# Kernel optimization log

Measured on AMD Instinct MI355X. Metric: run time of the kernel, lower is better.

Reference implementation:

```python
import jax, jax.numpy as jnp
import numpy as np

EMBED_DIM = 1024
NUM_HEADS = 16
NUM_KV_HEADS = 4
HEAD_DIM = 64
WINDOW_SIZE = 32
TOKENS_PER_FRAME = 64
BASE_T, BASE_D, BASE_B = 10000.0, 100.0, 100.0


def apply_3d_rope(x, pos_t, pos_d, pos_b):
    # x: (B, S, H, D); pos_*: (S,) int
    D = x.shape[-1]
    half = D // 2
    dim_idx = jnp.arange(half, dtype=jnp.float32)
    inv_freq = 1.0 / (BASE_T ** (2.0 * dim_idx / D))  # (half,)
    ang = (pos_t.astype(jnp.float32)[:, None] * inv_freq
           + pos_d.astype(jnp.float32)[:, None] * inv_freq * (BASE_T / BASE_D)
           + pos_b.astype(jnp.float32)[:, None] * inv_freq * (BASE_T / BASE_B))  # (S, half)
    cos = jnp.cos(ang)[None, :, None, :]
    sin = jnp.sin(ang)[None, :, None, :]
    x1 = x[..., 0::2]
    x2 = x[..., 1::2]
    y1 = x1 * cos - x2 * sin
    y2 = x1 * sin + x2 * cos
    return jnp.stack([y1, y2], axis=-1).reshape(x.shape)


def setup_inputs() -> dict:
    key = jax.random.key(0)
    ks = jax.random.split(key, 8)
    B, Sn, Lp = 1, 1024, 4096
    hidden_states = jax.random.normal(ks[0], (B, Sn, EMBED_DIM), dtype=jnp.float32)
    past_k = jax.random.normal(ks[1], (B, NUM_KV_HEADS, Lp, HEAD_DIM), dtype=jnp.float32)
    past_v = jax.random.normal(ks[2], (B, NUM_KV_HEADS, Lp, HEAD_DIM), dtype=jnp.float32)
    wq = jax.random.normal(ks[3], (EMBED_DIM, NUM_HEADS * HEAD_DIM), dtype=jnp.float32) * 0.02
    wk = jax.random.normal(ks[4], (EMBED_DIM, NUM_KV_HEADS * HEAD_DIM), dtype=jnp.float32) * 0.02
    wv = jax.random.normal(ks[5], (EMBED_DIM, NUM_KV_HEADS * HEAD_DIM), dtype=jnp.float32) * 0.02
    wo = jax.random.normal(ks[6], (NUM_HEADS * HEAD_DIM, EMBED_DIM), dtype=jnp.float32) * 0.02
    # frame-time positions: tokens_per_frame tokens share a frame time; past frames 0..63, new frames 64..79
    past_idx = jnp.arange(Lp, dtype=jnp.int32)
    new_idx = jnp.arange(Sn, dtype=jnp.int32)
    past_t = past_idx // TOKENS_PER_FRAME
    new_t = new_idx // TOKENS_PER_FRAME + Lp // TOKENS_PER_FRAME
    # 8x8 depth-by-bearing patch grid within each frame
    past_d = (past_idx % TOKENS_PER_FRAME) // 8
    past_b = past_idx % 8
    new_d = (new_idx % TOKENS_PER_FRAME) // 8
    new_b = new_idx % 8
    return dict(hidden_states=hidden_states, past_k=past_k, past_v=past_v,
                wq=wq, wk=wk, wv=wv, wo=wo,
                new_t=new_t, new_d=new_d, new_b=new_b,
                past_t=past_t, past_d=past_d, past_b=past_b)


def reference(hidden_states, past_k, past_v, wq, wk, wv, wo,
              new_t, new_d, new_b, past_t, past_d, past_b):
    B, Sn, _ = hidden_states.shape
    Lp = past_t.shape[0]
    Q = (hidden_states @ wq).reshape(B, Sn, NUM_HEADS, HEAD_DIM)
    Kn = (hidden_states @ wk).reshape(B, Sn, NUM_KV_HEADS, HEAD_DIM)
    Vn = (hidden_states @ wv).reshape(B, Sn, NUM_KV_HEADS, HEAD_DIM)
    Q = apply_3d_rope(Q, new_t, new_d, new_b)
    Kn = apply_3d_rope(Kn, new_t, new_d, new_b)
    Q = Q.transpose(0, 2, 1, 3)   # (B, H, Sn, D)
    Kn = Kn.transpose(0, 2, 1, 3)  # (B, KVH, Sn, D)
    Vn = Vn.transpose(0, 2, 1, 3)
    # Sliding-window truncation on frame time: torch does searchsorted + slice
    # (drop past keys with time < min_time). Masking those keys to -inf is
    # mathematically identical and jit-friendly (static shapes).
    min_time = new_t.max() - (WINDOW_SIZE - 1)
    past_keep = past_t >= min_time                                    # (Lp,)
    valid = jnp.concatenate([past_keep, jnp.ones((Sn,), dtype=bool)])  # (Lp+Sn,)
    pos_t = jnp.concatenate([past_t, new_t])
    K = jnp.concatenate([past_k, Kn], axis=2)  # (B, KVH, Lp+Sn, D)
    V = jnp.concatenate([past_v, Vn], axis=2)
    rep = NUM_HEADS // NUM_KV_HEADS
    K = jnp.repeat(K, rep, axis=1)  # (B, H, L, D) -- repeat_interleave semantics
    V = jnp.repeat(V, rep, axis=1)
    scores = jnp.einsum('bhqd,bhkd->bhqk', Q, K) / jnp.sqrt(jnp.float32(HEAD_DIM))
    mask = (pos_t[None, :] <= new_t[:, None]) & valid[None, :]  # (Sn, L) frame-causal + window
    scores = jnp.where(mask[None, None], scores, jnp.float32(-jnp.inf))
    attn = jax.nn.softmax(scores, axis=-1)
    attn = jnp.nan_to_num(attn)  # fully-masked rows -> 0 (matches torch nan_to_num)
    out = jnp.einsum('bhqk,bhkd->bhqd', attn, V)
    out = out.transpose(0, 2, 1, 3).reshape(B, Sn, NUM_HEADS * HEAD_DIM)
    out = out @ wo
    return out, Kn, Vn
```

## Files before the change

### kernel.cpp

```cpp
#include <hip/hip_runtime.h>
#include <math.h>

#define EMBED 1024
#define NH 16
#define NKV 4
#define HD 64
#define SN 1024
#define LP 4096
#define WIN 32

#define FREQ_C 0.4152410118609203f

typedef float floatx4 __attribute__((ext_vector_type(4)));
typedef __bf16 bf16x8 __attribute__((ext_vector_type(8)));

__global__ __launch_bounds__(256) void prep_kernel(
    const float* __restrict__ hidden, const float* __restrict__ wq,
    const float* __restrict__ wk, const float* __restrict__ wv,
    const float* __restrict__ wo,
    __bf16* __restrict__ hidb, __bf16* __restrict__ wqT,
    __bf16* __restrict__ wkT, __bf16* __restrict__ wvT,
    __bf16* __restrict__ woT)
{
    const int jb = blockIdx.x, tid = threadIdx.x;
    if (jb >= 640) {
        const size_t base = (size_t)(jb - 640) * 4096 + (size_t)tid * 16;
        float4 f0 = *(const float4*)(hidden + base);
        float4 f1 = *(const float4*)(hidden + base + 4);
        float4 f2 = *(const float4*)(hidden + base + 8);
        float4 f3 = *(const float4*)(hidden + base + 12);
        bf16x8 o0, o1;
        o0[0] = (__bf16)f0.x; o0[1] = (__bf16)f0.y;
        o0[2] = (__bf16)f0.z; o0[3] = (__bf16)f0.w;
        o0[4] = (__bf16)f1.x; o0[5] = (__bf16)f1.y;
        o0[6] = (__bf16)f1.z; o0[7] = (__bf16)f1.w;
        o1[0] = (__bf16)f2.x; o1[1] = (__bf16)f2.y;
        o1[2] = (__bf16)f2.z; o1[3] = (__bf16)f2.w;
        o1[4] = (__bf16)f3.x; o1[5] = (__bf16)f3.y;
        o1[6] = (__bf16)f3.z; o1[7] = (__bf16)f3.w;
        *(bf16x8*)(hidb + base) = o0;
        *(bf16x8*)(hidb + base + 8) = o1;
        return;
    }
    const float* src; __bf16* dst; int N, tk, tn;
    if (jb < 256)      { src = wq; dst = wqT; N = 1024; tk = jb >> 4;         tn = jb & 15; }
    else if (jb < 320) { src = wk; dst = wkT; N = 256;  tk = (jb - 256) >> 2; tn = (jb - 256) & 3; }
    else if (jb < 384) { src = wv; dst = wvT; N = 256;  tk = (jb - 320) >> 2; tn = (jb - 320) & 3; }
    else               { src = wo; dst = woT; N = 1024; tk = (jb - 384) >> 4; tn = (jb - 384) & 15; }

    __shared__ float T[64][65];
    {
        const int r = tid >> 2, c0 = (tid & 3) * 16;
        const float* sp = src + (size_t)(tk * 64 + r) * N + tn * 64 + c0;
        float4 v0 = *(const float4*)(sp + 0);
        float4 v1 = *(const float4*)(sp + 4);
        float4 v2 = *(const float4*)(sp + 8);
        float4 v3 = *(const float4*)(sp + 12);
        *(float4*)&T[r][c0 + 0] = v0;
        *(float4*)&T[r][c0 + 4] = v1;
        *(float4*)&T[r][c0 + 8] = v2;
        *(float4*)&T[r][c0 + 12] = v3;
    }
    __syncthreads();
    {
        const int n = tid >> 2, k0 = (tid & 3) * 16;
        bf16x8 o0, o1;
#pragma unroll
        for (int j = 0; j < 8; j++) {
            o0[j] = (__bf16)T[k0 + j][n];
            o1[j] = (__bf16)T[k0 + 8 + j][n];
        }
        __bf16* dp = dst + (size_t)(tn * 64 + n) * 1024 + tk * 64 + k0;
        *(bf16x8*)dp = o0;
        *(bf16x8*)(dp + 8) = o1;
    }
}

__global__ __launch_bounds__(256) void qkv_mfma_kernel(
    const __bf16* __restrict__ hidb, const __bf16* __restrict__ wqT,
    const __bf16* __restrict__ wkT, const __bf16* __restrict__ wvT,
    const int* __restrict__ new_t, const int* __restrict__ new_d,
    const int* __restrict__ new_b,
    float* __restrict__ qws, float* __restrict__ knp, float* __restrict__ vnp)
{
    __shared__ __bf16 ASh[64][72];
    __shared__ __bf16 BSh[64][72];

    const int tid = threadIdx.x;
    const int lane = tid & 63, w = tid >> 6;
    const int g = lane >> 4, c = lane & 15;
    const int bx = blockIdx.x, by = blockIdx.y;

    int mode, cbase;
    const __bf16* W;
    if (bx < 16)      { mode = 0; W = wqT; cbase = bx * 64; }
    else if (bx < 20) { mode = 1; W = wkT; cbase = (bx - 16) * 64; }
    else              { mode = 2; W = wvT; cbase = (bx - 20) * 64; }

    const int arow = tid >> 2, ak = (tid & 3) * 16;
    const __bf16* Ap = hidb + (size_t)(by * 64 + arow) * EMBED + ak;
    const int bn = tid & 63, bk0 = (tid >> 6) * 16;
    const __bf16* Bp = W + (size_t)(cbase + bn) * 1024 + bk0;

    floatx4 acc[4] = {floatx4(0.f), floatx4(0.f), floatx4(0.f), floatx4(0.f)};

    bf16x8 a0 = *(const bf16x8*)(Ap);
    bf16x8 a1 = *(const bf16x8*)(Ap + 8);
    bf16x8 b0 = *(const bf16x8*)(Bp);
    bf16x8 b1 = *(const bf16x8*)(Bp + 8);

    const int strip = w * 16;

    for (int k0 = 0; k0 < EMBED; k0 += 64) {
        __syncthreads();
        *(bf16x8*)&ASh[arow][ak] = a0;
        *(bf16x8*)&ASh[arow][ak + 8] = a1;
        *(bf16x8*)&BSh[bn][bk0] = b0;
        *(bf16x8*)&BSh[bn][bk0 + 8] = b1;
        __syncthreads();
        if (k0 + 64 < EMBED) {
            a0 = *(const bf16x8*)(Ap + k0 + 64);
            a1 = *(const bf16x8*)(Ap + k0 + 72);
            b0 = *(const bf16x8*)(Bp + k0 + 64);
            b1 = *(const bf16x8*)(Bp + k0 + 72);
        }
        bf16x8 af0 = *(const bf16x8*)&ASh[strip + c][g * 8];
        bf16x8 af1 = *(const bf16x8*)&ASh[strip + c][32 + g * 8];
#pragma unroll
        for (int t = 0; t < 4; t++) {
            bf16x8 bf0 = *(const bf16x8*)&BSh[t * 16 + c][g * 8];
            bf16x8 bf1 = *(const bf16x8*)&BSh[t * 16 + c][32 + g * 8];
            acc[t] = __builtin_amdgcn_mfma_f32_16x16x32_bf16(af0, bf0, acc[t], 0, 0, 0);
            acc[t] = __builtin_amdgcn_mfma_f32_16x16x32_bf16(af1, bf1, acc[t], 0, 0, 0);
        }
    }

    const int m0 = strip + g * 4;
    if (mode == 2) {
        const int kvh = bx - 20;
#pragma unroll
        for (int r = 0; r < 4; r++) {
            const int token = by * 64 + m0 + r;
#pragma unroll
            for (int t = 0; t < 4; t++)
                vnp[((size_t)kvh * SN + token) * HD + t * 16 + c] = acc[t][r];
        }
    } else {
        float fr[4];
#pragma unroll
        for (int t = 0; t < 4; t++) {
            const int d = (cbase + t * 16 + c) & 63;
            fr[t] = exp2f(-FREQ_C * (float)(d >> 1));
        }
        const int par = c & 1;
#pragma unroll
        for (int r = 0; r < 4; r++) {
            const int token = by * 64 + m0 + r;
            const float ft = (float)new_t[token];
            const float fdb = (float)(new_d[token] + new_b[token]);
#pragma unroll
            for (int t = 0; t < 4; t++) {
                const float ang = ft * fr[t] + fdb * (fr[t] * 100.0f);
                float sv, cv;
                sincosf(ang, &sv, &cv);
                const float x = acc[t][r];
                const float xp = __shfl_xor(x, 1, 64);
                const float y = par ? (xp * sv + x * cv) : (x * cv - xp * sv);
                if (mode == 0) {
                    qws[(size_t)token * EMBED + cbase + t * 16 + c] = y;
                } else {
                    const int kvh = bx - 16;
                    knp[((size_t)kvh * SN + token) * HD + t * 16 + c] = y;
                }
            }
        }
    }
}

__global__ __launch_bounds__(256) void out_mfma_kernel(
    const __bf16* __restrict__ ctxb, const __bf16* __restrict__ woT,
    float* __restrict__ C)
{
    __shared__ __bf16 ASh[64][72];
    __shared__ __bf16 BSh[64][72];

    const int tid = threadIdx.x;
    const int lane = tid & 63, w = tid >> 6;
    const int g = lane >> 4, c = lane & 15;
    const int bx = blockIdx.x, by = blockIdx.y;

    const int arow = tid >> 2, ak = (tid & 3) * 16;
    const __bf16* Ap = ctxb + (size_t)(by * 64 + arow) * EMBED + ak;
    const int bn = tid & 63, bk0 = (tid >> 6) * 16;
    const __bf16* Bp = woT + (size_t)(bx * 64 + bn) * 1024 + bk0;

    floatx4 acc[4] = {floatx4(0.f), floatx4(0.f), floatx4(0.f), floatx4(0.f)};

    bf16x8 a0 = *(const bf16x8*)(Ap);
    bf16x8 a1 = *(const bf16x8*)(Ap + 8);
    bf16x8 b0 = *(const bf16x8*)(Bp);
    bf16x8 b1 = *(const bf16x8*)(Bp + 8);

    const int strip = w * 16;

    for (int k0 = 0; k0 < EMBED; k0 += 64) {
        __syncthreads();
        *(bf16x8*)&ASh[arow][ak] = a0;
        *(bf16x8*)&ASh[arow][ak + 8] = a1;
        *(bf16x8*)&BSh[bn][bk0] = b0;
        *(bf16x8*)&BSh[bn][bk0 + 8] = b1;
        __syncthreads();
        if (k0 + 64 < EMBED) {
            a0 = *(const bf16x8*)(Ap + k0 + 64);
            a1 = *(const bf16x8*)(Ap + k0 + 72);
            b0 = *(const bf16x8*)(Bp + k0 + 64);
            b1 = *(const bf16x8*)(Bp + k0 + 72);
        }
        bf16x8 af0 = *(const bf16x8*)&ASh[strip + c][g * 8];
        bf16x8 af1 = *(const bf16x8*)&ASh[strip + c][32 + g * 8];
#pragma unroll
        for (int t = 0; t < 4; t++) {
            bf16x8 bf0 = *(const bf16x8*)&BSh[t * 16 + c][g * 8];
            bf16x8 bf1 = *(const bf16x8*)&BSh[t * 16 + c][32 + g * 8];
            acc[t] = __builtin_amdgcn_mfma_f32_16x16x32_bf16(af0, bf0, acc[t], 0, 0, 0);
            acc[t] = __builtin_amdgcn_mfma_f32_16x16x32_bf16(af1, bf1, acc[t], 0, 0, 0);
        }
    }

    const int m0 = strip + g * 4;
#pragma unroll
    for (int r = 0; r < 4; r++) {
        const int row = by * 64 + m0 + r;
#pragma unroll
        for (int t = 0; t < 4; t++)
            C[(size_t)row * EMBED + bx * 64 + t * 16 + c] = acc[t][r];
    }
}

#define PREFETCH_CHUNK(CI)                                                     \
    {                                                                          \
        const int base_ = (myStart + (CI)) << 6;                               \
        const int gk_ = base_ + skk;                                           \
        if (gk_ < Nk) {                                                        \
            const float* kp_ = (gk_ < nPast)                                   \
                ? past_k + ((size_t)(kvh * LP + p0 + gk_)) * HD + sd0          \
                : knp + ((size_t)(kvh * SN + (gk_ - nPast))) * HD + sd0;       \
            kb0 = *(const float4*)(kp_ + 0);                                   \
            kb1 = *(const float4*)(kp_ + 4);                                   \
            kb2 = *(const float4*)(kp_ + 8);                                   \
            kb3 = *(const float4*)(kp_ + 12);                                  \
        } else {                                                               \
            kb0 = kb1 = kb2 = kb3 = make_float4(0.f, 0.f, 0.f, 0.f);           \
        }                                                                      \
        const int gv0_ = base_ + 2 * kp2;                                      \
        if (gv0_ < Nk) {                                                       \
            const float* vp_ = (gv0_ < nPast)                                  \
                ? past_v + ((size_t)(kvh * LP + p0 + gv0_)) * HD + vdb         \
                : vnp + ((size_t)(kvh * SN + (gv0_ - nPast))) * HD + vdb;      \
            vb00 = *(const float4*)(vp_ + 0);                                  \
            vb01 = *(const float4*)(vp_ + 4);                                  \
        } else {                                                               \
            vb00 = vb01 = make_float4(0.f, 0.f, 0.f, 0.f);                     \
        }                                                                      \
        const int gv1_ = gv0_ + 1;                                             \
        if (gv1_ < Nk) {                                                       \
            const float* vp_ = (gv1_ < nPast)                                  \
                ? past_v + ((size_t)(kvh * LP + p0 + gv1_)) * HD + vdb         \
                : vnp + ((size_t)(kvh * SN + (gv1_ - nPast))) * HD + vdb;      \
            vb10 = *(const float4*)(vp_ + 0);                                  \
            vb11 = *(const float4*)(vp_ + 4);                                  \
        } else {                                                               \
            vb10 = vb11 = make_float4(0.f, 0.f, 0.f, 0.f);                     \
        }                                                                      \
        if (tid < 64) {                                                        \
            const int g2_ = base_ + tid;                                       \
            ptreg = (g2_ < Nk)                                                 \
                ? ((g2_ < nPast) ? past_t[p0 + g2_] : new_t[g2_ - nPast])      \
                : 0x7fffffff;                                                  \
        }                                                                      \
    }

__global__ __launch_bounds__(256) void attn_kernel(
    const float* __restrict__ qws, const float* __restrict__ past_k,
    const float* __restrict__ past_v, const float* __restrict__ knp,
    const float* __restrict__ vnp, const int* __restrict__ new_t,
    const int* __restrict__ past_t, float* __restrict__ opart,
    float* __restrict__ lpart)
{
    __shared__ __bf16 KS[64][72];
    __shared__ __bf16 VS[64][72];
    __shared__ __bf16 PS[64][72];
    __shared__ float MSK[64];

    const int tid = threadIdx.x;
    const int i = blockIdx.x;
    const int xcd = i & 7;
    const int kvh = xcd >> 1;
    const int jj = i >> 3;
    const int hloc = jj & 3;
    const int f = (jj >> 2) & 15;
    const int sidx = (xcd & 1) | (((jj >> 6) & 1) << 1);
    const int h = kvh * 4 + hloc;

    const int lane = tid & 63, w = tid >> 6;
    const int g = lane >> 4, c = lane & 15;

    const int tmax = new_t[SN - 1];
    const int min_time = tmax - (WIN - 1);
    const int qtf = new_t[f * 64];

    int lo = 0, hi = LP;
    while (lo < hi) {
        int mid = (lo + hi) >> 1;
        if (past_t[mid] >= min_time) hi = mid; else lo = mid + 1;
    }
    const int p0 = lo;
    const int nPast = LP - p0;
    const int Nk = nPast + (f + 1) * 64;

    const int nch = (Nk + 63) >> 6;
    const int qch = nch >> 2, rem = nch & 3;
    const int myCount = qch + (sidx < rem ? 1 : 0);
    const int myStart = sidx * qch + (sidx < rem ? sidx : rem);

    bf16x8 aQ[2];
    {
        const int q = f * 64 + w * 16 + c;
        const float* qp = qws + (size_t)q * EMBED + h * HD + g * 8;
#pragma unroll
        for (int s = 0; s < 2; s++) {
            float4 q0 = *(const float4*)(qp + s * 32);
            float4 q1 = *(const float4*)(qp + s * 32 + 4);
            bf16x8 a;
            a[0] = (__bf16)q0.x; a[1] = (__bf16)q0.y;
            a[2] = (__bf16)q0.z; a[3] = (__bf16)q0.w;
            a[4] = (__bf16)q1.x; a[5] = (__bf16)q1.y;
            a[6] = (__bf16)q1.z; a[7] = (__bf16)q1.w;
            aQ[s] = a;
        }
    }

    floatx4 oacc[4] = {floatx4(0.f), floatx4(0.f), floatx4(0.f), floatx4(0.f)};
    floatx4 lacc = floatx4(0.f);
    bf16x8 bOnes;
#pragma unroll
    for (int j = 0; j < 8; j++) bOnes[j] = (__bf16)1.0f;

    const float scale = 0.125f;

    const int skk = tid >> 2, sd0 = (tid & 3) * 16;
    const int kp2 = tid & 31, vdb = (tid >> 5) * 8;

    float4 kb0, kb1, kb2, kb3;
    float4 vb00, vb01, vb10, vb11;
    int ptreg = 0x7fffffff;

    if (myCount > 0) PREFETCH_CHUNK(0);

    for (int chi = 0; chi < myCount; ++chi) {
        __syncthreads();

        {
            bf16x8 t0, t1;
            t0[0] = (__bf16)kb0.x; t0[1] = (__bf16)kb0.y;
            t0[2] = (__bf16)kb0.z; t0[3] = (__bf16)kb0.w;
            t0[4] = (__bf16)kb1.x; t0[5] = (__bf16)kb1.y;
            t0[6] = (__bf16)kb1.z; t0[7] = (__bf16)kb1.w;
            t1[0] = (__bf16)kb2.x; t1[1] = (__bf16)kb2.y;
            t1[2] = (__bf16)kb2.z; t1[3] = (__bf16)kb2.w;
            t1[4] = (__bf16)kb3.x; t1[5] = (__bf16)kb3.y;
            t1[6] = (__bf16)kb3.z; t1[7] = (__bf16)kb3.w;
            *(bf16x8*)&KS[skk][sd0] = t0;
            *(bf16x8*)&KS[skk][sd0 + 8] = t1;
        }
        {
            float e0[8] = {vb00.x, vb00.y, vb00.z, vb00.w,
                           vb01.x, vb01.y, vb01.z, vb01.w};
            float e1[8] = {vb10.x, vb10.y, vb10.z, vb10.w,
                           vb11.x, vb11.y, vb11.z, vb11.w};
#pragma unroll
            for (int j = 0; j < 8; j++) {
                union { __bf16 b[2]; unsigned u; } pk;
                pk.b[0] = (__bf16)e0[j];
                pk.b[1] = (__bf16)e1[j];
                *(unsigned*)&VS[vdb + j][2 * kp2] = pk.u;
            }
        }
        if (tid < 64) {
            const int g2 = ((myStart + chi) << 6) + tid;
            const bool ok = (ptreg <= qtf) && ((g2 >= nPast) || (ptreg >= min_time));
            MSK[tid] = ok ? 0.f : -1e30f;
        }
        __syncthreads();

        if (chi + 1 < myCount) PREFETCH_CHUNK(chi + 1);

        floatx4 sacc[4];
#pragma unroll
        for (int t = 0; t < 4; t++) {
            sacc[t] = floatx4(0.f);
#pragma unroll
            for (int s = 0; s < 2; s++) {
                bf16x8 b = *(const bf16x8*)&KS[t * 16 + c][s * 32 + g * 8];
                sacc[t] = __builtin_amdgcn_mfma_f32_16x16x32_bf16(aQ[s], b, sacc[t], 0, 0, 0);
            }
        }

#pragma unroll
        for (int r = 0; r < 4; r++)
#pragma unroll
            for (int t = 0; t < 4; t++)
                PS[w * 16 + g * 4 + r][t * 16 + c] =
                    (__bf16)__expf(sacc[t][r] * scale + MSK[t * 16 + c]);

#pragma unroll
        for (int s = 0; s < 2; s++) {
            bf16x8 a = *(const bf16x8*)&PS[w * 16 + c][s * 32 + g * 8];
            lacc = __builtin_amdgcn_mfma_f32_16x16x32_bf16(a, bOnes, lacc, 0, 0, 0);
#pragma unroll
            for (int t = 0; t < 4; t++) {
                bf16x8 b = *(const bf16x8*)&VS[t * 16 + c][s * 32 + g * 8];
                oacc[t] = __builtin_amdgcn_mfma_f32_16x16x32_bf16(a, b, oacc[t], 0, 0, 0);
            }
        }
    }

    float* Op = opart + ((size_t)(f * 16 + h) * 4 + sidx) * 4096;
    float* lp = lpart + ((size_t)(f * 16 + h) * 4 + sidx) * 64;
#pragma unroll
    for (int r = 0; r < 4; r++) {
        const int q = w * 16 + g * 4 + r;
#pragma unroll
        for (int t = 0; t < 4; t++)
            Op[(size_t)q * 64 + t * 16 + c] = oacc[t][r];
        if (c == 0) lp[q] = lacc[r];
    }
}

__global__ __launch_bounds__(256) void attn_merge_kernel(
    const float* __restrict__ opart, const float* __restrict__ lpart,
    __bf16* __restrict__ ctxb)
{
    const int f = blockIdx.x, h = blockIdx.y;
    const int tid = threadIdx.x;
    const int q = tid >> 2, d0 = (tid & 3) * 16;
    const size_t fh = (size_t)(f * 16 + h);

    float l = 0.f;
#pragma unroll
    for (int s = 0; s < 4; s++) l += lpart[(fh * 4 + s) * 64 + q];
    const float inv = (l > 0.f) ? (1.f / l) : 0.f;

    float o[16] = {};
#pragma unroll
    for (int s = 0; s < 4; s++) {
        const float* Os = opart + (fh * 4 + s) * 4096 + (size_t)q * 64 + d0;
#pragma unroll
        for (int v = 0; v < 4; v++) {
            float4 ov = *(const float4*)(Os + v * 4);
            o[v * 4 + 0] += ov.x;
            o[v * 4 + 1] += ov.y;
            o[v * 4 + 2] += ov.z;
            o[v * 4 + 3] += ov.w;
        }
    }
    bf16x8 o0, o1;
#pragma unroll
    for (int j = 0; j < 8; j++) {
        o0[j] = (__bf16)(o[j] * inv);
        o1[j] = (__bf16)(o[8 + j] * inv);
    }
    __bf16* cp = ctxb + (size_t)(f * 64 + q) * EMBED + h * HD + d0;
    *(bf16x8*)cp = o0;
    *(bf16x8*)(cp + 8) = o1;
}

extern "C" void kernel_launch(void* const* d_in, const int* in_sizes, int n_in,
                              void* d_out, int out_size, void* d_ws, size_t ws_size,
                              hipStream_t stream) {
    const float* hidden = (const float*)d_in[0];
    const float* past_k = (const float*)d_in[1];
    const float* past_v = (const float*)d_in[2];
    const float* wq     = (const float*)d_in[3];
    const float* wk     = (const float*)d_in[4];
    const float* wv     = (const float*)d_in[5];
    const float* wo     = (const float*)d_in[6];
    const int* new_t    = (const int*)d_in[7];
    const int* new_d    = (const int*)d_in[8];
    const int* new_b    = (const int*)d_in[9];
    const int* past_t   = (const int*)d_in[10];

    float* out = (float*)d_out;
    float* knp = out + SN * EMBED;
    float* vnp = knp + NKV * SN * HD;

    float* qws   = (float*)d_ws;
    float* lpart = qws + (size_t)SN * EMBED;
    float* opart = lpart + (size_t)16 * 16 * 4 * 64;
    __bf16* hidb = (__bf16*)(opart + (size_t)16 * 16 * 4 * 4096);
    __bf16* wqT  = hidb + (size_t)SN * EMBED;
    __bf16* wkT  = wqT + (size_t)1024 * 1024;
    __bf16* wvT  = wkT + (size_t)256 * 1024;
    __bf16* woT  = wvT + (size_t)256 * 1024;
    __bf16* ctxb = woT + (size_t)1024 * 1024;

    prep_kernel<<<dim3(896), 256, 0, stream>>>(
        hidden, wq, wk, wv, wo, hidb, wqT, wkT, wvT, woT);
    qkv_mfma_kernel<<<dim3(24, 16), 256, 0, stream>>>(
        hidb, wqT, wkT, wvT, new_t, new_d, new_b, qws, knp, vnp);
    attn_kernel<<<dim3(1024), 256, 0, stream>>>(
        qws, past_k, past_v, knp, vnp, new_t, past_t, opart, lpart);
    attn_merge_kernel<<<dim3(16, 16), 256, 0, stream>>>(opart, lpart, ctxb);
    out_mfma_kernel<<<dim3(16, 16), 256, 0, stream>>>(ctxb, woT, out);
}
```

Baseline: 155.1 us.

## Halve GEMM M-tile to 32 rows and store Q workspace as bf16

Both the QKV projection and output projection GEMMs now use 32x64 output tiles instead of 64x64, with four warps arranged 2x2 and each warp computing two 16x16 tiles. This doubles the grid (384 to 768 and 256 to 512 blocks) so more of the GPU's CUs are busy. Separately, the rotated Q is written to the workspace as bf16 rather than fp32, halving that write and letting the attention kernel load Q fragments directly without converting. Smaller tiles reload the weight tile more often and do less MFMA work per shared-memory load.

New measurement: 151.8 us. 2.1% less time.

```diff
diff --git a/kernel.cpp b/kernel.cpp
--- a/kernel.cpp
+++ b/kernel.cpp
@@ -81,9 +81,9 @@
     const __bf16* __restrict__ wkT, const __bf16* __restrict__ wvT,
     const int* __restrict__ new_t, const int* __restrict__ new_d,
     const int* __restrict__ new_b,
-    float* __restrict__ qws, float* __restrict__ knp, float* __restrict__ vnp)
+    __bf16* __restrict__ qws, float* __restrict__ knp, float* __restrict__ vnp)
 {
-    __shared__ __bf16 ASh[64][72];
+    __shared__ __bf16 ASh[32][72];
     __shared__ __bf16 BSh[64][72];
 
     const int tid = threadIdx.x;
@@ -97,80 +97,80 @@
     else if (bx < 20) { mode = 1; W = wkT; cbase = (bx - 16) * 64; }
     else              { mode = 2; W = wvT; cbase = (bx - 20) * 64; }
 
-    const int arow = tid >> 2, ak = (tid & 3) * 16;
-    const __bf16* Ap = hidb + (size_t)(by * 64 + arow) * EMBED + ak;
+    const int arow = tid >> 3, ak = (tid & 7) * 8;
+    const __bf16* Ap = hidb + (size_t)(by * 32 + arow) * EMBED + ak;
     const int bn = tid & 63, bk0 = (tid >> 6) * 16;
     const __bf16* Bp = W + (size_t)(cbase + bn) * 1024 + bk0;
 
-    floatx4 acc[4] = {floatx4(0.f), floatx4(0.f), floatx4(0.f), floatx4(0.f)};
+    floatx4 acc[2] = {floatx4(0.f), floatx4(0.f)};
 
     bf16x8 a0 = *(const bf16x8*)(Ap);
-    bf16x8 a1 = *(const bf16x8*)(Ap + 8);
     bf16x8 b0 = *(const bf16x8*)(Bp);
     bf16x8 b1 = *(const bf16x8*)(Bp + 8);
 
-    const int strip = w * 16;
+    const int mt = (w & 1) * 16;
+    const int nt0 = (w >> 1) * 2;
 
     for (int k0 = 0; k0 < EMBED; k0 += 64) {
         __syncthreads();
         *(bf16x8*)&ASh[arow][ak] = a0;
-        *(bf16x8*)&ASh[arow][ak + 8] = a1;
         *(bf16x8*)&BSh[bn][bk0] = b0;
         *(bf16x8*)&BSh[bn][bk0 + 8] = b1;
         __syncthreads();
         if (k0 + 64 < EMBED) {
             a0 = *(const bf16x8*)(Ap + k0 + 64);
-            a1 = *(const bf16x8*)(Ap + k0 + 72);
             b0 = *(const bf16x8*)(Bp + k0 + 64);
             b1 = *(const bf16x8*)(Bp + k0 + 72);
         }
-        bf16x8 af0 = *(const bf16x8*)&ASh[strip + c][g * 8];
-        bf16x8 af1 = *(const bf16x8*)&ASh[strip + c][32 + g * 8];
-#pragma unroll
-        for (int t = 0; t < 4; t++) {
-            bf16x8 bf0 = *(const bf16x8*)&BSh[t * 16 + c][g * 8];
-            bf16x8 bf1 = *(const bf16x8*)&BSh[t * 16 + c][32 + g * 8];
+        bf16x8 af0 = *(const bf16x8*)&ASh[mt + c][g * 8];
+        bf16x8 af1 = *(const bf16x8*)&ASh[mt + c][32 + g * 8];
+#pragma unroll
+        for (int t = 0; t < 2; t++) {
+            const int tn = nt0 + t;
+            bf16x8 bf0 = *(const bf16x8*)&BSh[tn * 16 + c][g * 8];
+            bf16x8 bf1 = *(const bf16x8*)&BSh[tn * 16 + c][32 + g * 8];
             acc[t] = __builtin_amdgcn_mfma_f32_16x16x32_bf16(af0, bf0, acc[t], 0, 0, 0);
             acc[t] = __builtin_amdgcn_mfma_f32_16x16x32_bf16(af1, bf1, acc[t], 0, 0, 0);
         }
     }
 
-    const int m0 = strip + g * 4;
+    const int m0 = mt + g * 4;
     if (mode == 2) {
         const int kvh = bx - 20;
 #pragma unroll
         for (int r = 0; r < 4; r++) {
-            const int token = by * 64 + m0 + r;
-#pragma unroll
-            for (int t = 0; t < 4; t++)
-                vnp[((size_t)kvh * SN + token) * HD + t * 16 + c] = acc[t][r];
+            const int token = by * 32 + m0 + r;
+#pragma unroll
+            for (int t = 0; t < 2; t++)
+                vnp[((size_t)kvh * SN + token) * HD + (nt0 + t) * 16 + c] = acc[t][r];
         }
     } else {
-        float fr[4];
-#pragma unroll
-        for (int t = 0; t < 4; t++) {
-            const int d = (cbase + t * 16 + c) & 63;
+        float fr[2];
+#pragma unroll
+        for (int t = 0; t < 2; t++) {
+            const int d = (cbase + (nt0 + t) * 16 + c) & 63;
             fr[t] = exp2f(-FREQ_C * (float)(d >> 1));
         }
         const int par = c & 1;
 #pragma unroll
         for (int r = 0; r < 4; r++) {
-            const int token = by * 64 + m0 + r;
+            const int token = by * 32 + m0 + r;
             const float ft = (float)new_t[token];
             const float fdb = (float)(new_d[token] + new_b[token]);
 #pragma unroll
-            for (int t = 0; t < 4; t++) {
+            for (int t = 0; t < 2; t++) {
                 const float ang = ft * fr[t] + fdb * (fr[t] * 100.0f);
                 float sv, cv;
                 sincosf(ang, &sv, &cv);
                 const float x = acc[t][r];
                 const float xp = __shfl_xor(x, 1, 64);
                 const float y = par ? (xp * sv + x * cv) : (x * cv - xp * sv);
+                const int col = cbase + (nt0 + t) * 16 + c;
                 if (mode == 0) {
-                    qws[(size_t)token * EMBED + cbase + t * 16 + c] = y;
+                    qws[(size_t)token * EMBED + col] = (__bf16)y;
                 } else {
                     const int kvh = bx - 16;
-                    knp[((size_t)kvh * SN + token) * HD + t * 16 + c] = y;
+                    knp[((size_t)kvh * SN + token) * HD + (col & 63)] = y;
                 }
             }
         }
@@ -181,7 +181,7 @@
     const __bf16* __restrict__ ctxb, const __bf16* __restrict__ woT,
     float* __restrict__ C)
 {
-    __shared__ __bf16 ASh[64][72];
+    __shared__ __bf16 ASh[32][72];
     __shared__ __bf16 BSh[64][72];
 
     const int tid = threadIdx.x;
@@ -189,51 +189,50 @@
     const int g = lane >> 4, c = lane & 15;
     const int bx = blockIdx.x, by = blockIdx.y;
 
-    const int arow = tid >> 2, ak = (tid & 3) * 16;
-    const __bf16* Ap = ctxb + (size_t)(by * 64 + arow) * EMBED + ak;
+    const int arow = tid >> 3, ak = (tid & 7) * 8;
+    const __bf16* Ap = ctxb + (size_t)(by * 32 + arow) * EMBED + ak;
     const int bn = tid & 63, bk0 = (tid >> 6) * 16;
     const __bf16* Bp = woT + (size_t)(bx * 64 + bn) * 1024 + bk0;
 
-    floatx4 acc[4] = {floatx4(0.f), floatx4(0.f), floatx4(0.f), floatx4(0.f)};
+    floatx4 acc[2] = {floatx4(0.f), floatx4(0.f)};
 
     bf16x8 a0 = *(const bf16x8*)(Ap);
-    bf16x8 a1 = *(const bf16x8*)(Ap + 8);
     bf16x8 b0 = *(const bf16x8*)(Bp);
     bf16x8 b1 = *(const bf16x8*)(Bp + 8);
 
-    const int strip = w * 16;
+    const int mt = (w & 1) * 16;
+    const int nt0 = (w >> 1) * 2;
 
     for (int k0 = 0; k0 < EMBED; k0 += 64) {
         __syncthreads();
         *(bf16x8*)&ASh[arow][ak] = a0;
-        *(bf16x8*)&ASh[arow][ak + 8] = a1;
         *(bf16x8*)&BSh[bn][bk0] = b0;
         *(bf16x8*)&BSh[bn][bk0 + 8] = b1;
         __syncthreads();
         if (k0 + 64 < EMBED) {
             a0 = *(const bf16x8*)(Ap + k0 + 64);
-            a1 = *(const bf16x8*)(Ap + k0 + 72);
             b0 = *(const bf16x8*)(Bp + k0 + 64);
             b1 = *(const bf16x8*)(Bp + k0 + 72);
         }
-        bf16x8 af0 = *(const bf16x8*)&ASh[strip + c][g * 8];
-        bf16x8 af1 = *(const bf16x8*)&ASh[strip + c][32 + g * 8];
-#pragma unroll
-        for (int t = 0; t < 4; t++) {
-            bf16x8 bf0 = *(const bf16x8*)&BSh[t * 16 + c][g * 8];
-            bf16x8 bf1 = *(const bf16x8*)&BSh[t * 16 + c][32 + g * 8];
+        bf16x8 af0 = *(const bf16x8*)&ASh[mt + c][g * 8];
+        bf16x8 af1 = *(const bf16x8*)&ASh[mt + c][32 + g * 8];
+#pragma unroll
+        for (int t = 0; t < 2; t++) {
+            const int tn = nt0 + t;
+            bf16x8 bf0 = *(const bf16x8*)&BSh[tn * 16 + c][g * 8];
+            bf16x8 bf1 = *(const bf16x8*)&BSh[tn * 16 + c][32 + g * 8];
             acc[t] = __builtin_amdgcn_mfma_f32_16x16x32_bf16(af0, bf0, acc[t], 0, 0, 0);
             acc[t] = __builtin_amdgcn_mfma_f32_16x16x32_bf16(af1, bf1, acc[t], 0, 0, 0);
         }
     }
 
-    const int m0 = strip + g * 4;
+    const int m0 = mt + g * 4;
 #pragma unroll
     for (int r = 0; r < 4; r++) {
-        const int row = by * 64 + m0 + r;
-#pragma unroll
-        for (int t = 0; t < 4; t++)
-            C[(size_t)row * EMBED + bx * 64 + t * 16 + c] = acc[t][r];
+        const int row = by * 32 + m0 + r;
+#pragma unroll
+        for (int t = 0; t < 2; t++)
+            C[(size_t)row * EMBED + bx * 64 + (nt0 + t) * 16 + c] = acc[t][r];
     }
 }
 
@@ -281,7 +280,7 @@
     }
 
 __global__ __launch_bounds__(256) void attn_kernel(
-    const float* __restrict__ qws, const float* __restrict__ past_k,
+    const __bf16* __restrict__ qws, const float* __restrict__ past_k,
     const float* __restrict__ past_v, const float* __restrict__ knp,
     const float* __restrict__ vnp, const int* __restrict__ new_t,
     const int* __restrict__ past_t, float* __restrict__ opart,
@@ -326,18 +325,9 @@
     bf16x8 aQ[2];
     {
         const int q = f * 64 + w * 16 + c;
-        const float* qp = qws + (size_t)q * EMBED + h * HD + g * 8;
-#pragma unroll
-        for (int s = 0; s < 2; s++) {
-            float4 q0 = *(const float4*)(qp + s * 32);
-            float4 q1 = *(const float4*)(qp + s * 32 + 4);
-            bf16x8 a;
-            a[0] = (__bf16)q0.x; a[1] = (__bf16)q0.y;
-            a[2] = (__bf16)q0.z; a[3] = (__bf16)q0.w;
-            a[4] = (__bf16)q1.x; a[5] = (__bf16)q1.y;
-            a[6] = (__bf16)q1.z; a[7] = (__bf16)q1.w;
-            aQ[s] = a;
-        }
+        const __bf16* qp = qws + (size_t)q * EMBED + h * HD + g * 8;
+        aQ[0] = *(const bf16x8*)(qp);
+        aQ[1] = *(const bf16x8*)(qp + 32);
     }
 
     floatx4 oacc[4] = {floatx4(0.f), floatx4(0.f), floatx4(0.f), floatx4(0.f)};
@@ -494,10 +484,10 @@
     float* knp = out + SN * EMBED;
     float* vnp = knp + NKV * SN * HD;
 
-    float* qws   = (float*)d_ws;
-    float* lpart = qws + (size_t)SN * EMBED;
+    float* lpart = (float*)d_ws;
     float* opart = lpart + (size_t)16 * 16 * 4 * 64;
-    __bf16* hidb = (__bf16*)(opart + (size_t)16 * 16 * 4 * 4096);
+    __bf16* qws  = (__bf16*)(opart + (size_t)16 * 16 * 4 * 4096);
+    __bf16* hidb = qws + (size_t)SN * EMBED;
     __bf16* wqT  = hidb + (size_t)SN * EMBED;
     __bf16* wkT  = wqT + (size_t)1024 * 1024;
     __bf16* wvT  = wkT + (size_t)256 * 1024;
@@ -506,10 +496,10 @@
 
     prep_kernel<<<dim3(896), 256, 0, stream>>>(
         hidden, wq, wk, wv, wo, hidb, wqT, wkT, wvT, woT);
-    qkv_mfma_kernel<<<dim3(24, 16), 256, 0, stream>>>(
+    qkv_mfma_kernel<<<dim3(24, 32), 256, 0, stream>>>(
         hidb, wqT, wkT, wvT, new_t, new_d, new_b, qws, knp, vnp);
     attn_kernel<<<dim3(1024), 256, 0, stream>>>(
         qws, past_k, past_v, knp, vnp, new_t, past_t, opart, lpart);
     attn_merge_kernel<<<dim3(16, 16), 256, 0, stream>>>(opart, lpart, ctxb);
-    out_mfma_kernel<<<dim3(16, 16), 256, 0, stream>>>(ctxb, woT, out);
+    out_mfma_kernel<<<dim3(16, 32), 256, 0, stream>>>(ctxb, woT, out);
 }
```
